# Kernel optimization log

Measured on AMD Instinct MI355X. Metric: run time of the kernel, lower is better.

The kernel has to match this reference:

```python
import jax, jax.numpy as jnp
import numpy as np

EMBED_DIM = 1024
NUM_HEADS = 16
HEAD_DIM = EMBED_DIM // NUM_HEADS
B, S = 4, 2048


def setup_inputs() -> dict:
    key = jax.random.key(0)
    ks = jax.random.split(key, 11)
    d = EMBED_DIM
    s = 1.0 / np.sqrt(d)
    return {
        "query": jax.random.normal(ks[0], (B, S, d), jnp.float32),
        "key": jax.random.normal(ks[1], (B, S, d), jnp.float32),
        "value": jax.random.normal(ks[2], (B, S, d), jnp.float32),
        "Wq": jax.random.normal(ks[3], (d, d), jnp.float32) * s,
        "bq": jnp.zeros((d,), jnp.float32),
        "Wk": jax.random.normal(ks[4], (d, d), jnp.float32) * s,
        "bk": jnp.zeros((d,), jnp.float32),
        "Wv": jax.random.normal(ks[5], (d, d), jnp.float32) * s,
        "bv": jnp.zeros((d,), jnp.float32),
        "Wo": jax.random.normal(ks[6], (d, d), jnp.float32) * s,
        "bo": jnp.zeros((d,), jnp.float32),
    }


def reference(query, key, value, Wq, bq, Wk, bk, Wv, bv, Wo, bo):
    b, t, d = query.shape
    s = key.shape[1]
    h, hd = NUM_HEADS, HEAD_DIM
    # Linear projections (torch Linear: x @ W.T + b)
    q = (query @ Wq.T + bq).reshape(b, t, h, hd).transpose(0, 2, 1, 3)  # [B,H,T,hd]
    k = (key @ Wk.T + bk).reshape(b, s, h, hd).transpose(0, 2, 1, 3)    # [B,H,S,hd]
    v = (value @ Wv.T + bv).reshape(b, s, h, hd).transpose(0, 2, 1, 3)  # [B,H,S,hd]
    scale = 1.0 / np.sqrt(hd).astype(np.float32)
    attn = jnp.einsum('bhtd,bhsd->bhts', q, k) * scale  # [B,H,T,S]
    attn = jax.nn.softmax(attn, axis=-1)
    out = jnp.einsum('bhts,bhsd->bhtd', attn, v)        # [B,H,T,hd]
    out = out.transpose(0, 2, 1, 3).reshape(b, t, d)    # [B,T,D]
    out = out @ Wo.T + bo
    return out
```

## Files before the change

### kernel.cpp

```cpp
#include <hip/hip_runtime.h>
#include <hip/hip_bf16.h>
#include <stdint.h>

typedef __attribute__((ext_vector_type(8))) short short8;
typedef __attribute__((ext_vector_type(4))) float floatx4;
typedef __attribute__((ext_vector_type(16))) float floatx16;
typedef __attribute__((ext_vector_type(4))) uint16_t ushort4v;

#define MFMA16(a, b, c) __builtin_amdgcn_mfma_f32_16x16x32_bf16((a), (b), (c), 0, 0, 0)
#define MFMA32(a, b, c) __builtin_amdgcn_mfma_f32_32x32x16_bf16((a), (b), (c), 0, 0, 0)

#define GLOAD_LDS16(g, l)                                                          \
  __builtin_amdgcn_global_load_lds(                                                \
      (const __attribute__((address_space(1))) uint32_t*)(g),                      \
      (__attribute__((address_space(3))) uint32_t*)(l), 16, 0, 0)

#define CVTPK(lo_, hi_, out_) \
  asm("v_cvt_pk_bf16_f32 %0, %1, %2" : "=v"(out_) : "v"(lo_), "v"(hi_))
#define SWAP32(a_, b_) \
  asm("v_permlane32_swap_b32 %0, %1" : "+v"(a_), "+v"(b_))

__device__ __forceinline__ uint16_t f2bf(float x) {
  union { float f; uint32_t u; } c; c.f = x;
  return (uint16_t)((c.u + 0x7FFFu + ((c.u >> 16) & 1u)) >> 16);
}

__global__ void cvt3_k(const float* __restrict__ s0, const float* __restrict__ s1,
                       const float* __restrict__ s2, uint16_t* __restrict__ dst, int n4) {
  const float* src = blockIdx.z == 0 ? s0 : (blockIdx.z == 1 ? s1 : s2);
  uint16_t* d = dst + (size_t)blockIdx.z * 8388608;
  int stride = gridDim.x * blockDim.x;
  for (int i = blockIdx.x * blockDim.x + threadIdx.x; i < n4; i += stride) {
    float4 v = ((const float4*)src)[i];
    ushort4v o;
    o.x = f2bf(v.x); o.y = f2bf(v.y); o.z = f2bf(v.z); o.w = f2bf(v.w);
    ((ushort4v*)d)[i] = o;
  }
}
__global__ void cvt4_k(const float* __restrict__ s0, const float* __restrict__ s1,
                       const float* __restrict__ s2, const float* __restrict__ s3,
                       uint16_t* __restrict__ dst, int n4) {
  const float* src = blockIdx.z == 0 ? s0 : (blockIdx.z == 1 ? s1 : (blockIdx.z == 2 ? s2 : s3));
  uint16_t* d = dst + (size_t)blockIdx.z * 1048576;
  int stride = gridDim.x * blockDim.x;
  for (int i = blockIdx.x * blockDim.x + threadIdx.x; i < n4; i += stride) {
    float4 v = ((const float4*)src)[i];
    ushort4v o;
    o.x = f2bf(v.x); o.y = f2bf(v.y); o.z = f2bf(v.z); o.w = f2bf(v.w);
    ((ushort4v*)d)[i] = o;
  }
}

template <int OUT_BF16>
__device__ __forceinline__ void gemm_body(const uint16_t* __restrict__ A,
                                          const uint16_t* __restrict__ W,
                                          const float* __restrict__ bias,
                                          void* __restrict__ Cout, float scale) {
  constexpr int N = 1024, K = 1024;
  __shared__ uint16_t As[128 * 32];
  __shared__ uint16_t Bs[128 * 32];
  const int t = threadIdx.x;
  const int l = t & 63;
  const int w = t >> 6;
  const int wr = w >> 1, wc = w & 1;
  const int l16 = l & 15, lhi = l >> 4;
  const int brow = blockIdx.y * 128;
  const int bcol = blockIdx.x * 128;

  floatx4 acc[4][4] = {};

  for (int k0 = 0; k0 < K; k0 += 32) {
#pragma unroll
    for (int j = 0; j < 2; ++j) {
      int c = j * 256 + t;
      int row = c >> 2;
      int ko = (c & 3) * 8;
      const uint16_t* ga = A + (size_t)(brow + row) * K + k0 + ko;
      const uint16_t* gb = W + (size_t)(bcol + row) * K + k0 + ko;
      uint16_t* la = As + (size_t)(j * 256 + w * 64) * 8;
      uint16_t* lb = Bs + (size_t)(j * 256 + w * 64) * 8;
      GLOAD_LDS16(ga, la);
      GLOAD_LDS16(gb, lb);
    }
    __syncthreads();

    short8 a[4], b[4];
#pragma unroll
    for (int m = 0; m < 4; ++m)
      a[m] = *(const short8*)&As[(wr * 64 + m * 16 + l16) * 32 + lhi * 8];
#pragma unroll
    for (int n = 0; n < 4; ++n)
      b[n] = *(const short8*)&Bs[(wc * 64 + n * 16 + l16) * 32 + lhi * 8];
#pragma unroll
    for (int m = 0; m < 4; ++m)
#pragma unroll
      for (int n = 0; n < 4; ++n)
        acc[m][n] = MFMA16(a[m], b[n], acc[m][n]);
    __syncthreads();
  }

#pragma unroll
  for (int n = 0; n < 4; ++n) {
    int col = bcol + wc * 64 + n * 16 + l16;
    float bv = bias[col];
#pragma unroll
    for (int m = 0; m < 4; ++m) {
#pragma unroll
      for (int j = 0; j < 4; ++j) {
        int row = brow + wr * 64 + m * 16 + lhi * 4 + j;
        float v = (acc[m][n][j] + bv) * scale;
        if (OUT_BF16)
          ((uint16_t*)Cout)[(size_t)row * N + col] = f2bf(v);
        else
          ((float*)Cout)[(size_t)row * N + col] = v;
      }
    }
  }
}

__global__ __launch_bounds__(256)
void gemm_qkv_k(const uint16_t* __restrict__ XQ, const uint16_t* __restrict__ XK,
                const uint16_t* __restrict__ XV, const uint16_t* __restrict__ WQ,
                const uint16_t* __restrict__ WK, const uint16_t* __restrict__ WV,
                const float* __restrict__ bq, const float* __restrict__ bk,
                const float* __restrict__ bv, uint16_t* __restrict__ QP,
                uint16_t* __restrict__ KP, uint16_t* __restrict__ VP, float qscale) {
  const uint16_t *A, *W; const float* bi; uint16_t* C; float sc;
  if (blockIdx.z == 0)      { A = XQ; W = WQ; bi = bq; C = QP; sc = qscale; }
  else if (blockIdx.z == 1) { A = XK; W = WK; bi = bk; C = KP; sc = 1.0f; }
  else                      { A = XV; W = WV; bi = bv; C = VP; sc = 1.0f; }
  gemm_body<1>(A, W, bi, C, sc);
}

__global__ __launch_bounds__(256)
void gemm_o_k(const uint16_t* __restrict__ A, const uint16_t* __restrict__ W,
              const float* __restrict__ bias, float* __restrict__ Cout) {
  gemm_body<0>(A, W, bias, Cout, 1.0f);
}

__global__ __launch_bounds__(256)
void vtrans_k(const uint16_t* __restrict__ VP, uint16_t* __restrict__ VT) {
  __shared__ uint16_t T[64][66];
  const int t = threadIdx.x;
  const int bh = blockIdx.y;
  const int s0 = blockIdx.x * 64;
  const int b = bh >> 4, h = bh & 15;
  const size_t src = ((size_t)b * 2048 + s0) * 1024 + (size_t)h * 64;
#pragma unroll
  for (int it = 0; it < 2; ++it) {
    int u = it * 256 + t;
    int s = u >> 3;
    int d0 = (u & 7) * 8;
    short8 v = *(const short8*)(VP + src + (size_t)s * 1024 + d0);
#pragma unroll
    for (int i = 0; i < 8; ++i) T[s][d0 + i] = (uint16_t)v[i];
  }
  __syncthreads();
  const size_t dst = (size_t)bh * 131072 + s0;
#pragma unroll
  for (int it = 0; it < 2; ++it) {
    int u = it * 256 + t;
    int d = u >> 3;
    int ss = (u & 7) * 8;
    union { uint16_t u16[8]; short8 s8; } pk;
#pragma unroll
    for (int i = 0; i < 8; ++i) pk.u16[i] = T[ss + i][d];
    *(short8*)(VT + dst + (size_t)d * 2048 + ss) = pk.s8;
  }
}

__global__ __launch_bounds__(512, 2)
void attn_k(const uint16_t* __restrict__ Qp, const uint16_t* __restrict__ Kp,
            const uint16_t* __restrict__ Vt, uint16_t* __restrict__ AO) {
  __shared__ uint16_t Kl[2][64 * 128];
  __shared__ uint16_t Vl[2][64 * 128];

  const int t = threadIdx.x;
  const int l = t & 63, w = t >> 6;
  const int l32 = l & 31, hi = l >> 5;

  const int f = blockIdx.y * 8 + blockIdx.x;
  const int virt = (f & 7) * 64 + (f >> 3);
  const int vx = virt & 7;
  const int vy = virt >> 3;

  const int q0 = vx * 256 + w * 32;
  const size_t base = (size_t)(vy >> 4) * 2048 * 1024 + (size_t)(vy & 15) * 64;
  const size_t vbg = (size_t)vy * 131072;

  union PAu { uint32_t u[4]; short8 s; };

  const uint16_t* pK[2];
  const uint16_t* pV[2];
#pragma unroll
  for (int i = 0; i < 2; ++i) {
    int c = i * 512 + t;
    int r = c >> 4, qs = c & 15;
    int q0c = qs ^ (r & 15);
    pK[i] = Kp + base + (size_t)(64 * (q0c >> 3) + r) * 1024 + (q0c & 7) * 8;
    pV[i] = Vt + vbg + (size_t)r * 2048 + q0c * 8;
  }

#define STAGE_ALL(NB)                                                 \
  {                                                                   \
    _Pragma("unroll") for (int i = 0; i < 2; ++i) {                   \
      GLOAD_LDS16(pK[i], &Kl[NB][(size_t)(i * 512 + w * 64) * 8]);    \
      GLOAD_LDS16(pV[i], &Vl[NB][(size_t)(i * 512 + w * 64) * 8]);    \
      pK[i] += 131072;                          \
      pV[i] += 128;                              \
    }                                                                 \
  }

  short8 qf[4];
#pragma unroll
  for (int ks = 0; ks < 4; ++ks)
    qf[ks] = *(const short8*)(Qp + base + (size_t)(q0 + l32) * 1024 + ks * 16 + hi * 8);

  floatx16 of0 = {}, of1 = {};
  float rs = 0.f;

  const int swzb = (l32 & 15);
  const int krow = l32 * 256;

  STAGE_ALL(0);
  __syncthreads();

#define HALF(CUR, H)                                                                  \
  {                                                                                   \
    floatx16 sf0 = {}, sf1 = {};                                                      \
    __builtin_amdgcn_s_setprio(1);                                                    \
    _Pragma("unroll") for (int ks = 0; ks < 4; ++ks) {                                \
      int kbyte = krow + (((H * 8 + 2 * ks + hi) ^ swzb) << 4);                       \
      short8 kf0 = *(const short8*)((char*)Kl[CUR] + kbyte);                          \
      short8 kf1 = *(const short8*)((char*)Kl[CUR] + kbyte + 8192);                   \
      sf0 = MFMA32(kf0, qf[ks], sf0);                                                 \
      sf1 = MFMA32(kf1, qf[ks], sf1);                                                 \
    }                                                                                 \
    __builtin_amdgcn_s_setprio(0);                                                    \
    _Pragma("unroll") for (int r = 0; r < 16; ++r) {                                  \
      sf0[r] = __builtin_amdgcn_exp2f(sf0[r]);                                        \
      sf1[r] = __builtin_amdgcn_exp2f(sf1[r]);                                        \
      rs += sf0[r] + sf1[r];                                                          \
    }                                                                                 \
    PAu pa[4];                                                                        \
    _Pragma("unroll") for (int sb = 0; sb < 2; ++sb) {                                \
      const floatx16& sv = sb ? sf1 : sf0;                                            \
      _Pragma("unroll") for (int ks = 0; ks < 2; ++ks) {                              \
        uint32_t a0, a1, b0, b1;                                                      \
        CVTPK(sv[8 * ks + 0], sv[8 * ks + 1], a0);                                    \
        CVTPK(sv[8 * ks + 2], sv[8 * ks + 3], a1);                                    \
        CVTPK(sv[8 * ks + 4], sv[8 * ks + 5], b0);                                    \
        CVTPK(sv[8 * ks + 6], sv[8 * ks + 7], b1);                                    \
        SWAP32(a0, b0);                                                               \
        SWAP32(a1, b1);                                                               \
        pa[sb * 2 + ks].u[0] = a0; pa[sb * 2 + ks].u[1] = a1;                         \
        pa[sb * 2 + ks].u[2] = b0; pa[sb * 2 + ks].u[3] = b1;                         \
      }                                                                               \
    }                                                                                 \
    __builtin_amdgcn_s_setprio(1);                                                    \
    _Pragma("unroll") for (int kk = 0; kk < 4; ++kk) {                                \
      int vbyte = krow + (((H * 8 + 2 * kk + hi) ^ swzb) << 4);                       \
      short8 vf0 = *(const short8*)((char*)Vl[CUR] + vbyte);                          \
      short8 vf1 = *(const short8*)((char*)Vl[CUR] + vbyte + 8192);                   \
      of0 = MFMA32(pa[kk].s, vf0, of0);                                               \
      of1 = MFMA32(pa[kk].s, vf1, of1);                                               \
    }                                                                                 \
    __builtin_amdgcn_s_setprio(0);                                                    \
  }

#define STEP128(CUR, PF)                                                              \
  {                                                                                   \
    if (PF) STAGE_ALL(CUR ^ 1);                                                       \
    HALF(CUR, 0);                                                                     \
    HALF(CUR, 1);                                                                     \
    __syncthreads();                                                                  \
  }

  for (int it = 0; it < 8; ++it) {
    STEP128(0, 1);
    STEP128(1, it < 7);
  }

  rs += __shfl_xor(rs, 32);
#pragma unroll
  for (int r = 0; r < 16; ++r) {
    int qloc = (r & 3) + 8 * (r >> 2) + 4 * hi;
    float rsq = __shfl(rs, qloc);
    float rinv = 1.0f / rsq;
    int qrow = q0 + qloc;
    AO[base + (size_t)qrow * 1024 + l32]      = f2bf(of0[r] * rinv);
    AO[base + (size_t)qrow * 1024 + 32 + l32] = f2bf(of1[r] * rinv);
  }
#undef STAGE_ALL
#undef HALF
#undef STEP128
}

extern "C" void kernel_launch(void* const* d_in, const int* in_sizes, int n_in,
                              void* d_out, int out_size, void* d_ws, size_t ws_size,
                              hipStream_t stream) {
  const float* q  = (const float*)d_in[0];
  const float* k  = (const float*)d_in[1];
  const float* v  = (const float*)d_in[2];
  const float* Wq = (const float*)d_in[3];
  const float* bq = (const float*)d_in[4];
  const float* Wk = (const float*)d_in[5];
  const float* bk = (const float*)d_in[6];
  const float* Wv = (const float*)d_in[7];
  const float* bv = (const float*)d_in[8];
  const float* Wo = (const float*)d_in[9];
  const float* bo = (const float*)d_in[10];

  const size_t MB = 1ull << 20;
  char* ws = (char*)d_ws;
  uint16_t* XQ  = (uint16_t*)(ws + 0 * MB);
  uint16_t* XK  = (uint16_t*)(ws + 16 * MB);
  uint16_t* XV  = (uint16_t*)(ws + 32 * MB);
  uint16_t* WQb = (uint16_t*)(ws + 48 * MB);
  uint16_t* WKb = (uint16_t*)(ws + 50 * MB);
  uint16_t* WVb = (uint16_t*)(ws + 52 * MB);
  uint16_t* WOb = (uint16_t*)(ws + 54 * MB);
  uint16_t* QP  = (uint16_t*)(ws + 56 * MB);
  uint16_t* KP  = (uint16_t*)(ws + 72 * MB);
  uint16_t* VP  = (uint16_t*)(ws + 88 * MB);
  uint16_t* AO  = XQ;
  uint16_t* VT  = XK;

  const int NTOK = 4 * 2048;
  const int D = 1024;
  const int nBig = NTOK * D / 4;
  const int nW = D * D / 4;
  const float qscale = 0.125f * 1.4426950408889634f;

  cvt3_k<<<dim3(2048, 1, 3), dim3(256), 0, stream>>>(q, k, v, XQ, nBig);
  cvt4_k<<<dim3(1024, 1, 4), dim3(256), 0, stream>>>(Wq, Wk, Wv, Wo, WQb, nW);

  gemm_qkv_k<<<dim3(D / 128, NTOK / 128, 3), dim3(256), 0, stream>>>(
      XQ, XK, XV, WQb, WKb, WVb, bq, bk, bv, QP, KP, VP, qscale);

  vtrans_k<<<dim3(32, 64), dim3(256), 0, stream>>>(VP, VT);

  attn_k<<<dim3(8, 64), dim3(512), 0, stream>>>(QP, KP, VT, AO);

  gemm_o_k<<<dim3(D / 128, NTOK / 128), dim3(256), 0, stream>>>(AO, WOb, bo, (float*)d_out);
}
```

Measured before the change: 212.3 us.

## Software-pipeline QK, softmax and PV across 32-key quarters within each step

Splits each 128-key step into four 32-key quarters and interleaves them so the QK MFMAs for the next quarter are issued before the exp/pack and PV MFMAs of the previous quarter. The aim is to overlap transcendental and conversion VALU work with matrix-core work instead of running them as serial phases. It also drops the s_setprio hints. The two live score accumulators add register pressure.

```diff
diff --git a/kernel.cpp b/kernel.cpp
--- a/kernel.cpp
+++ b/kernel.cpp
@@ -207,7 +207,7 @@
       GLOAD_LDS16(pK[i], &Kl[NB][(size_t)(i * 512 + w * 64) * 8]);    \
       GLOAD_LDS16(pV[i], &Vl[NB][(size_t)(i * 512 + w * 64) * 8]);    \
       pK[i] += 131072;                          \
-      pV[i] += 128;                              \
+      pV[i] += 128;                             \
     }                                                                 \
   }
 
@@ -225,54 +225,76 @@
   STAGE_ALL(0);
   __syncthreads();
 
-#define HALF(CUR, H)                                                                  \
+#define QK_Q(SF, CUR, H, RH)                                                          \
   {                                                                                   \
-    floatx16 sf0 = {}, sf1 = {};                                                      \
-    __builtin_amdgcn_s_setprio(1);                                                    \
     _Pragma("unroll") for (int ks = 0; ks < 4; ++ks) {                                \
-      int kbyte = krow + (((H * 8 + 2 * ks + hi) ^ swzb) << 4);                       \
-      short8 kf0 = *(const short8*)((char*)Kl[CUR] + kbyte);                          \
-      short8 kf1 = *(const short8*)((char*)Kl[CUR] + kbyte + 8192);                   \
-      sf0 = MFMA32(kf0, qf[ks], sf0);                                                 \
-      sf1 = MFMA32(kf1, qf[ks], sf1);                                                 \
-    }                                                                                 \
-    __builtin_amdgcn_s_setprio(0);                                                    \
+      int kbyte = krow + (RH) * 8192 + ((((H) * 8 + 2 * ks + hi) ^ swzb) << 4);       \
+      short8 kf = *(const short8*)((char*)Kl[CUR] + kbyte);                           \
+      SF = MFMA32(kf, qf[ks], SF);                                                    \
+    }                                                                                 \
+  }
+
+#define EXPPACK(SF, P0, P1)                                                           \
+  {                                                                                   \
     _Pragma("unroll") for (int r = 0; r < 16; ++r) {                                  \
-      sf0[r] = __builtin_amdgcn_exp2f(sf0[r]);                                        \
-      sf1[r] = __builtin_amdgcn_exp2f(sf1[r]);                                        \
-      rs += sf0[r] + sf1[r];                                                          \
-    }                                                                                 \
-    PAu pa[4];                                                                        \
-    _Pragma("unroll") for (int sb = 0; sb < 2; ++sb) {                                \
-      const floatx16& sv = sb ? sf1 : sf0;                                            \
-      _Pragma("unroll") for (int ks = 0; ks < 2; ++ks) {                              \
-        uint32_t a0, a1, b0, b1;                                                      \
-        CVTPK(sv[8 * ks + 0], sv[8 * ks + 1], a0);                                    \
-        CVTPK(sv[8 * ks + 2], sv[8 * ks + 3], a1);                                    \
-        CVTPK(sv[8 * ks + 4], sv[8 * ks + 5], b0);                                    \
-        CVTPK(sv[8 * ks + 6], sv[8 * ks + 7], b1);                                    \
-        SWAP32(a0, b0);                                                               \
-        SWAP32(a1, b1);                                                               \
-        pa[sb * 2 + ks].u[0] = a0; pa[sb * 2 + ks].u[1] = a1;                         \
-        pa[sb * 2 + ks].u[2] = b0; pa[sb * 2 + ks].u[3] = b1;                         \
-      }                                                                               \
-    }                                                                                 \
-    __builtin_amdgcn_s_setprio(1);                                                    \
-    _Pragma("unroll") for (int kk = 0; kk < 4; ++kk) {                                \
-      int vbyte = krow + (((H * 8 + 2 * kk + hi) ^ swzb) << 4);                       \
-      short8 vf0 = *(const short8*)((char*)Vl[CUR] + vbyte);                          \
-      short8 vf1 = *(const short8*)((char*)Vl[CUR] + vbyte + 8192);                   \
-      of0 = MFMA32(pa[kk].s, vf0, of0);                                               \
-      of1 = MFMA32(pa[kk].s, vf1, of1);                                               \
-    }                                                                                 \
-    __builtin_amdgcn_s_setprio(0);                                                    \
+      SF[r] = __builtin_amdgcn_exp2f(SF[r]);                                          \
+      rs += SF[r];                                                                    \
+    }                                                                                 \
+    uint32_t a0, a1, b0, b1;                                                          \
+    CVTPK(SF[0], SF[1], a0); CVTPK(SF[2], SF[3], a1);                                 \
+    CVTPK(SF[4], SF[5], b0); CVTPK(SF[6], SF[7], b1);                                 \
+    SWAP32(a0, b0); SWAP32(a1, b1);                                                   \
+    P0.u[0] = a0; P0.u[1] = a1; P0.u[2] = b0; P0.u[3] = b1;                           \
+    CVTPK(SF[8], SF[9], a0); CVTPK(SF[10], SF[11], a1);                               \
+    CVTPK(SF[12], SF[13], b0); CVTPK(SF[14], SF[15], b1);                             \
+    SWAP32(a0, b0); SWAP32(a1, b1);                                                   \
+    P1.u[0] = a0; P1.u[1] = a1; P1.u[2] = b0; P1.u[3] = b1;                           \
+  }
+
+#define PV_Q(P0, P1, CUR, H, RH)                                                      \
+  {                                                                                   \
+    int vb0 = krow + ((((H) * 8 + 2 * (2 * (RH)) + hi) ^ swzb) << 4);                 \
+    int vb1 = krow + ((((H) * 8 + 2 * (2 * (RH) + 1) + hi) ^ swzb) << 4);             \
+    short8 vf00 = *(const short8*)((char*)Vl[CUR] + vb0);                             \
+    short8 vf01 = *(const short8*)((char*)Vl[CUR] + vb0 + 8192);                      \
+    short8 vf10 = *(const short8*)((char*)Vl[CUR] + vb1);                             \
+    short8 vf11 = *(const short8*)((char*)Vl[CUR] + vb1 + 8192);                      \
+    of0 = MFMA32(P0.s, vf00, of0);                                                    \
+    of1 = MFMA32(P0.s, vf01, of1);                                                    \
+    of0 = MFMA32(P1.s, vf10, of0);                                                    \
+    of1 = MFMA32(P1.s, vf11, of1);                                                    \
   }
 
 #define STEP128(CUR, PF)                                                              \
   {                                                                                   \
     if (PF) STAGE_ALL(CUR ^ 1);                                                       \
-    HALF(CUR, 0);                                                                     \
-    HALF(CUR, 1);                                                                     \
+    floatx16 sfA = {}, sfB = {};                                                      \
+    QK_Q(sfA, CUR, 0, 0);                                              \
+    QK_Q(sfB, CUR, 0, 1);                              \
+    {                                                                                 \
+      PAu p0, p1;                                                                     \
+      EXPPACK(sfA, p0, p1);                                                           \
+      PV_Q(p0, p1, CUR, 0, 0);                                                        \
+    }                                                                                 \
+    sfA = (floatx16){};                                                               \
+    QK_Q(sfA, CUR, 1, 0);                                    \
+    {                                                                                 \
+      PAu p0, p1;                                                                     \
+      EXPPACK(sfB, p0, p1);                                                           \
+      PV_Q(p0, p1, CUR, 0, 1);                                                        \
+    }                                                                                 \
+    sfB = (floatx16){};                                                               \
+    QK_Q(sfB, CUR, 1, 1);                                    \
+    {                                                                                 \
+      PAu p0, p1;                                                                     \
+      EXPPACK(sfA, p0, p1);                                                           \
+      PV_Q(p0, p1, CUR, 1, 0);                                                        \
+    }                                                                                 \
+    {                                                                                 \
+      PAu p0, p1;                                                                     \
+      EXPPACK(sfB, p0, p1);                                                           \
+      PV_Q(p0, p1, CUR, 1, 1);                                                        \
+    }                                                                                 \
     __syncthreads();                                                                  \
   }
 
@@ -292,7 +314,9 @@
     AO[base + (size_t)qrow * 1024 + 32 + l32] = f2bf(of1[r] * rinv);
   }
 #undef STAGE_ALL
-#undef HALF
+#undef QK_Q
+#undef EXPPACK
+#undef PV_Q
 #undef STEP128
 }
 
```

After: 217.2 us. 1.02x slower.
